# Kernel tuning notes

Hardware: AMD Instinct MI355X
Metric: run time of the kernel (lower is better)

The kernel has to match this reference:

```python
import jax, jax.numpy as jnp
import numpy as np

EPS = 1e-5

def _bn(x, gamma, beta):
    # BatchNorm1d in training mode: batch stats with biased variance
    m = jnp.mean(x, axis=0)
    v = jnp.mean((x - m) ** 2, axis=0)
    return (x - m) * jax.lax.rsqrt(v + EPS) * gamma + beta

def setup_inputs() -> dict:
    key = jax.random.key(0)
    ks = jax.random.split(key, 10)
    E, G = 500000, 512
    D_NODE, D_EDGE, D_U, OUT = 128, 64, 64, 256
    D_IN = 2 * D_NODE + D_EDGE + D_U  # 384
    return {
        "src": jax.random.normal(ks[0], (E, D_NODE), jnp.float32),
        "dest": jax.random.normal(ks[1], (E, D_NODE), jnp.float32),
        "edge_attr": jax.random.normal(ks[2], (E, D_EDGE), jnp.float32),
        "u": jax.random.normal(ks[3], (G, D_U), jnp.float32),
        "batch": jax.random.randint(ks[4], (E,), 0, G, jnp.int64),
        "W1": jax.random.normal(ks[5], (D_IN, OUT), jnp.float32) * (1.0 / np.sqrt(D_IN)),
        "g1": jnp.ones((OUT,), jnp.float32),
        "b1": jnp.zeros((OUT,), jnp.float32),
        "W2": jax.random.normal(ks[6], (OUT, OUT), jnp.float32) * (1.0 / np.sqrt(OUT)),
        "g2": jnp.ones((OUT,), jnp.float32),
        "b2": jnp.zeros((OUT,), jnp.float32),
    }

def reference(src, dest, edge_attr, u, batch, W1, g1, b1, W2, g2, b2):
    # gather per-graph globals to edges, concat features: [E, 384]
    h = jnp.concatenate([src, dest, edge_attr, u[batch]], axis=1)
    h = jax.nn.relu(_bn(h @ W1, g1, b1))  # LinearNorm + ReLU
    return _bn(h @ W2, g2, b2)            # LinearNorm
```

## Files before the change

kernel.cpp:

```cpp
#include <hip/hip_runtime.h>
#include <stdint.h>

typedef __attribute__((ext_vector_type(8))) short short8;
typedef __attribute__((ext_vector_type(4))) float float4v;

#define BM 128
#define BN 128
#define BK 32
#define LDT 40

__device__ __forceinline__ unsigned short f2bf(float f) {
    union { float f; unsigned u; } x; x.f = f;
    unsigned u = x.u;
    u += 0x7fffu + ((u >> 16) & 1u);
    return (unsigned short)(u >> 16);
}
__device__ __forceinline__ float bf2f(unsigned short s) {
    union { unsigned u; float f; } x; x.u = ((unsigned)s) << 16;
    return x.f;
}

__global__ __launch_bounds__(256) void transpose_bf16_kernel(
    const float* __restrict__ W, unsigned short* __restrict__ WT, int K, int N)
{
    int idx = blockIdx.x * 256 + threadIdx.x;
    if (idx < K * N) {
        int k = idx / N, n = idx - k * N;
        WT[(size_t)n * K + k] = f2bf(W[idx]);
    }
}

__global__ __launch_bounds__(256) void gemm1_kernel(
    const float* __restrict__ src, const float* __restrict__ dst,
    const float* __restrict__ edge, const float* __restrict__ u,
    const int* __restrict__ batch, const unsigned short* __restrict__ W1T,
    unsigned short* __restrict__ H1, float* __restrict__ psum,
    float* __restrict__ psq, int E, int MT)
{
    __shared__ __align__(16) unsigned short lsA[BM * LDT];
    __shared__ __align__(16) unsigned short lsB[BN * LDT];
    __shared__ int lsBatch[BM];
    __shared__ float ldsS[4][64];
    __shared__ float ldsQ[4][64];

    const int t = threadIdx.x;
    const int bm = blockIdx.x, bn = blockIdx.y;
    const int lane = t & 63, w = t >> 6;
    const int wm = w >> 1, wn = w & 1;
    const int quad = lane >> 4, l16 = lane & 15;

    if (t < BM) {
        int grow = bm * BM + t; if (grow >= E) grow = E - 1;
        lsBatch[t] = batch[grow];
    }

    float4v acc[4][4] = {};

    const int tc = t & 7, tr0 = t >> 3;
    const int kq = (t & 3) * 8, nb = t >> 2;
    const int n0 = bn * BN;

    for (int kk = 0; kk < 12; kk++) {
        const int kc = kk * BK;
        #pragma unroll
        for (int i = 0; i < 4; i++) {
            int rl = tr0 + 32 * i;
            int grow = bm * BM + rl; if (grow >= E) grow = E - 1;
            const float* p;
            if (kk < 4)       p = src  + (size_t)grow * 128 + kc + tc * 4;
            else if (kk < 8)  p = dst  + (size_t)grow * 128 + (kc - 128) + tc * 4;
            else if (kk < 10) p = edge + (size_t)grow * 64  + (kc - 256) + tc * 4;
            else              p = u + (size_t)lsBatch[rl] * 64 + (kc - 320) + tc * 4;
            float4v v = *(const float4v*)p;
            unsigned short* dp = &lsA[rl * LDT + tc * 4];
            dp[0] = f2bf(v[0]); dp[1] = f2bf(v[1]); dp[2] = f2bf(v[2]); dp[3] = f2bf(v[3]);
        }
        #pragma unroll
        for (int i = 0; i < 2; i++) {
            int n = nb + 64 * i;
            short8 v = *(const short8*)(W1T + (size_t)(n0 + n) * 384 + kc + kq);
            *(short8*)&lsB[n * LDT + kq] = v;
        }
        __syncthreads();
        short8 af[4], bfv[4];
        #pragma unroll
        for (int x = 0; x < 4; x++) {
            af[x]  = *(const short8*)&lsA[(wm * 64 + x * 16 + l16) * LDT + quad * 8];
            bfv[x] = *(const short8*)&lsB[(wn * 64 + x * 16 + l16) * LDT + quad * 8];
        }
        #pragma unroll
        for (int i = 0; i < 4; i++)
            #pragma unroll
            for (int j = 0; j < 4; j++)
                acc[i][j] = __builtin_amdgcn_mfma_f32_16x16x32_bf16(af[i], bfv[j], acc[i][j], 0, 0, 0);
        __syncthreads();
    }

    float s[4] = {0.f,0.f,0.f,0.f}, q[4] = {0.f,0.f,0.f,0.f};
    #pragma unroll
    for (int i = 0; i < 4; i++) {
        #pragma unroll
        for (int r = 0; r < 4; r++) {
            int row = bm * BM + wm * 64 + i * 16 + quad * 4 + r;
            bool ok = row < E;
            #pragma unroll
            for (int j = 0; j < 4; j++) {
                float v = acc[i][j][r];
                int col = bn * BN + wn * 64 + j * 16 + l16;
                if (ok) {
                    H1[(size_t)row * 256 + col] = f2bf(v);
                    s[j] += v; q[j] += v * v;
                }
            }
        }
    }
    #pragma unroll
    for (int j = 0; j < 4; j++) {
        s[j] += __shfl_xor(s[j], 16, 64); s[j] += __shfl_xor(s[j], 32, 64);
        q[j] += __shfl_xor(q[j], 16, 64); q[j] += __shfl_xor(q[j], 32, 64);
    }
    if (quad == 0) {
        #pragma unroll
        for (int j = 0; j < 4; j++) { ldsS[w][j * 16 + l16] = s[j]; ldsQ[w][j * 16 + l16] = q[j]; }
    }
    __syncthreads();
    if (t < 128) {
        int g = t >> 6, i = t & 63;
        float S = ldsS[g][i] + ldsS[g + 2][i];
        float Q = ldsQ[g][i] + ldsQ[g + 2][i];
        int col = bn * BN + t;
        psum[(size_t)col * MT + bm] = S;
        psq [(size_t)col * MT + bm] = Q;
    }
}

__global__ __launch_bounds__(256) void stats_kernel(
    const float* __restrict__ psum, const float* __restrict__ psq,
    const float* __restrict__ gamma, const float* __restrict__ beta,
    float* __restrict__ ad, int MT, float invE)
{
    __shared__ float rs[4], rq[4];
    int c = blockIdx.x;
    float s = 0.f, q = 0.f;
    for (int i = threadIdx.x; i < MT; i += 256) {
        s += psum[(size_t)c * MT + i];
        q += psq [(size_t)c * MT + i];
    }
    for (int off = 32; off >= 1; off >>= 1) {
        s += __shfl_xor(s, off, 64);
        q += __shfl_xor(q, off, 64);
    }
    int lane = threadIdx.x & 63, w = threadIdx.x >> 6;
    if (lane == 0) { rs[w] = s; rq[w] = q; }
    __syncthreads();
    if (threadIdx.x == 0) {
        float S = rs[0] + rs[1] + rs[2] + rs[3];
        float Q = rq[0] + rq[1] + rq[2] + rq[3];
        float m = S * invE;
        float v = Q * invE - m * m;
        float a = gamma[c] * rsqrtf(v + 1e-5f);
        ad[c] = a;
        ad[256 + c] = beta[c] - m * a;
    }
}

__global__ __launch_bounds__(256) void gemm2_kernel(
    const unsigned short* __restrict__ H1, const unsigned short* __restrict__ W2T,
    const float* __restrict__ ad1, float* __restrict__ out,
    float* __restrict__ psum, float* __restrict__ psq, int E, int MT)
{
    __shared__ __align__(16) unsigned short lsA[BM * LDT];
    __shared__ __align__(16) unsigned short lsB[BN * LDT];
    __shared__ float ldsS[4][64];
    __shared__ float ldsQ[4][64];

    const int t = threadIdx.x;
    const int bm = blockIdx.x, bn = blockIdx.y;
    const int lane = t & 63, w = t >> 6;
    const int wm = w >> 1, wn = w & 1;
    const int quad = lane >> 4, l16 = lane & 15;

    float4v acc[4][4] = {};

    const int kq = (t & 3) * 8, rb = t >> 2;
    const int n0 = bn * BN;

    for (int kk = 0; kk < 8; kk++) {
        const int kc = kk * BK;
        float4v aLo = *(const float4v*)(ad1 + kc + kq);
        float4v aHi = *(const float4v*)(ad1 + kc + kq + 4);
        float4v dLo = *(const float4v*)(ad1 + 256 + kc + kq);
        float4v dHi = *(const float4v*)(ad1 + 256 + kc + kq + 4);
        #pragma unroll
        for (int i = 0; i < 2; i++) {
            int rl = rb + 64 * i;
            int grow = bm * BM + rl; if (grow >= E) grow = E - 1;
            short8 hv = *(const short8*)(H1 + (size_t)grow * 256 + kc + kq);
            short8 yv;
            #pragma unroll
            for (int e = 0; e < 4; e++) {
                float y = fmaxf(fmaf(bf2f((unsigned short)hv[e]), aLo[e], dLo[e]), 0.f);
                yv[e] = (short)f2bf(y);
            }
            #pragma unroll
            for (int e = 0; e < 4; e++) {
                float y = fmaxf(fmaf(bf2f((unsigned short)hv[4 + e]), aHi[e], dHi[e]), 0.f);
                yv[4 + e] = (short)f2bf(y);
            }
            *(short8*)&lsA[rl * LDT + kq] = yv;
        }
        #pragma unroll
        for (int i = 0; i < 2; i++) {
            int n = rb + 64 * i;
            short8 v = *(const short8*)(W2T + (size_t)(n0 + n) * 256 + kc + kq);
            *(short8*)&lsB[n * LDT + kq] = v;
        }
        __syncthreads();
        short8 af[4], bfv[4];
        #pragma unroll
        for (int x = 0; x < 4; x++) {
            af[x]  = *(const short8*)&lsA[(wm * 64 + x * 16 + l16) * LDT + quad * 8];
            bfv[x] = *(const short8*)&lsB[(wn * 64 + x * 16 + l16) * LDT + quad * 8];
        }
        #pragma unroll
        for (int i = 0; i < 4; i++)
            #pragma unroll
            for (int j = 0; j < 4; j++)
                acc[i][j] = __builtin_amdgcn_mfma_f32_16x16x32_bf16(af[i], bfv[j], acc[i][j], 0, 0, 0);
        __syncthreads();
    }

    float s[4] = {0.f,0.f,0.f,0.f}, q[4] = {0.f,0.f,0.f,0.f};
    #pragma unroll
    for (int i = 0; i < 4; i++) {
        #pragma unroll
        for (int r = 0; r < 4; r++) {
            int row = bm * BM + wm * 64 + i * 16 + quad * 4 + r;
            bool ok = row < E;
            #pragma unroll
            for (int j = 0; j < 4; j++) {
                float v = acc[i][j][r];
                int col = bn * BN + wn * 64 + j * 16 + l16;
                if (ok) {
                    out[(size_t)row * 256 + col] = v;
                    s[j] += v; q[j] += v * v;
                }
            }
        }
    }
    #pragma unroll
    for (int j = 0; j < 4; j++) {
        s[j] += __shfl_xor(s[j], 16, 64); s[j] += __shfl_xor(s[j], 32, 64);
        q[j] += __shfl_xor(q[j], 16, 64); q[j] += __shfl_xor(q[j], 32, 64);
    }
    if (quad == 0) {
        #pragma unroll
        for (int j = 0; j < 4; j++) { ldsS[w][j * 16 + l16] = s[j]; ldsQ[w][j * 16 + l16] = q[j]; }
    }
    __syncthreads();
    if (t < 128) {
        int g = t >> 6, i = t & 63;
        float S = ldsS[g][i] + ldsS[g + 2][i];
        float Q = ldsQ[g][i] + ldsQ[g + 2][i];
        int col = bn * BN + t;
        psum[(size_t)col * MT + bm] = S;
        psq [(size_t)col * MT + bm] = Q;
    }
}

__global__ __launch_bounds__(256) void finalize_kernel(
    float* __restrict__ out, const float* __restrict__ ad, long n4)
{
    long stride = (long)gridDim.x * 256;
    for (long i = (long)blockIdx.x * 256 + threadIdx.x; i < n4; i += stride) {
        float4v v = ((float4v*)out)[i];
        int c4 = (int)(i & 63);
        float4v a = ((const float4v*)ad)[c4];
        float4v d = ((const float4v*)(ad + 256))[c4];
        v = a * v + d;
        ((float4v*)out)[i] = v;
    }
}

extern "C" void kernel_launch(void* const* d_in, const int* in_sizes, int n_in,
                              void* d_out, int out_size, void* d_ws, size_t ws_size,
                              hipStream_t stream)
{
    const float* src  = (const float*)d_in[0];
    const float* dst  = (const float*)d_in[1];
    const float* edge = (const float*)d_in[2];
    const float* u    = (const float*)d_in[3];
    const int*   batch= (const int*)d_in[4];
    const float* W1   = (const float*)d_in[5];
    const float* g1   = (const float*)d_in[6];
    const float* b1   = (const float*)d_in[7];
    const float* W2   = (const float*)d_in[8];
    const float* g2   = (const float*)d_in[9];
    const float* b2   = (const float*)d_in[10];
    float* out = (float*)d_out;

    const int E  = in_sizes[0] / 128;
    const int MT = (E + BM - 1) / BM;

    char* ws = (char*)d_ws;
    size_t off = 0;
    auto alloc = [&](size_t bytes) -> void* {
        void* p = (void*)(ws + off);
        off += (bytes + 255) & ~(size_t)255;
        return p;
    };
    unsigned short* H1  = (unsigned short*)alloc((size_t)E * 256 * 2);
    unsigned short* W1T = (unsigned short*)alloc((size_t)256 * 384 * 2);
    unsigned short* W2T = (unsigned short*)alloc((size_t)256 * 256 * 2);
    float* psum = (float*)alloc((size_t)256 * MT * 4);
    float* psq  = (float*)alloc((size_t)256 * MT * 4);
    float* ad1  = (float*)alloc(512 * 4);
    float* ad2  = (float*)alloc(512 * 4);
    (void)ws_size; (void)n_in; (void)out_size;

    transpose_bf16_kernel<<<(384 * 256 + 255) / 256, 256, 0, stream>>>(W1, W1T, 384, 256);
    transpose_bf16_kernel<<<(256 * 256 + 255) / 256, 256, 0, stream>>>(W2, W2T, 256, 256);
    gemm1_kernel<<<dim3(MT, 2), 256, 0, stream>>>(src, dst, edge, u, batch, W1T, H1, psum, psq, E, MT);
    stats_kernel<<<256, 256, 0, stream>>>(psum, psq, g1, b1, ad1, MT, 1.0f / (float)E);
    gemm2_kernel<<<dim3(MT, 2), 256, 0, stream>>>(H1, W2T, ad1, out, psum, psq, E, MT);
    stats_kernel<<<256, 256, 0, stream>>>(psum, psq, g2, b2, ad2, MT, 1.0f / (float)E);
    const long n4 = (long)E * 64;
    finalize_kernel<<<16384, 256, 0, stream>>>(out, ad2, n4);
}
```

Measured before the change: 1.525 ms.

## Double-buffer A tiles and load B fragments directly from global in both GEMMs

Both GEMM kernels now prefetch the next K-slice of A (and W) into registers while MFMAs run on the current slice. The A tile sits in a double-buffered LDS array, so only one barrier per iteration is needed instead of two. The B operand no longer goes through LDS: each wave reads its MFMA fragments straight from global memory. A-tile stores are packed into 64-bit writes. This hides global-load latency behind compute, at the cost of more registers and uncoalesced, repeated per-wave global reads of the weights.

New measurement: 1.607 ms. 5.4% more time.

```diff
diff --git a/kernel.cpp b/kernel.cpp
--- a/kernel.cpp
+++ b/kernel.cpp
@@ -3,6 +3,7 @@
 
 typedef __attribute__((ext_vector_type(8))) short short8;
 typedef __attribute__((ext_vector_type(4))) float float4v;
+typedef __attribute__((ext_vector_type(2))) unsigned int uint2v;
 
 #define BM 128
 #define BN 128
@@ -37,8 +38,7 @@
     unsigned short* __restrict__ H1, float* __restrict__ psum,
     float* __restrict__ psq, int E, int MT)
 {
-    __shared__ __align__(16) unsigned short lsA[BM * LDT];
-    __shared__ __align__(16) unsigned short lsB[BN * LDT];
+    __shared__ __align__(16) unsigned short lsA[2][BM * LDT];
     __shared__ int lsBatch[BM];
     __shared__ float ldsS[4][64];
     __shared__ float ldsQ[4][64];
@@ -57,43 +57,78 @@
     float4v acc[4][4] = {};
 
     const int tc = t & 7, tr0 = t >> 3;
-    const int kq = (t & 3) * 8, nb = t >> 2;
     const int n0 = bn * BN;
-
+    const unsigned short* Bbase = W1T + (size_t)(n0 + wn * 64 + l16) * 384 + quad * 8;
+
+    float4v aCur[4]; short8 bCur[4];
+
+    #pragma unroll
+    for (int i = 0; i < 4; i++) {
+        int rl = tr0 + 32 * i;
+        int grow = bm * BM + rl; if (grow >= E) grow = E - 1;
+        aCur[i] = *(const float4v*)(src + (size_t)grow * 128 + tc * 4);
+    }
+    #pragma unroll
+    for (int x = 0; x < 4; x++)
+        bCur[x] = *(const short8*)(Bbase + (size_t)x * 16 * 384);
+    #pragma unroll
+    for (int i = 0; i < 4; i++) {
+        int rl = tr0 + 32 * i;
+        unsigned lo = (unsigned)f2bf(aCur[i][0]) | ((unsigned)f2bf(aCur[i][1]) << 16);
+        unsigned hi = (unsigned)f2bf(aCur[i][2]) | ((unsigned)f2bf(aCur[i][3]) << 16);
+        uint2v v2; v2.x = lo; v2.y = hi;
+        *(uint2v*)&lsA[0][rl * LDT + tc * 4] = v2;
+    }
+    __syncthreads();
+
+    int cur = 0;
+    #pragma unroll 1
     for (int kk = 0; kk < 12; kk++) {
-        const int kc = kk * BK;
-        #pragma unroll
-        for (int i = 0; i < 4; i++) {
-            int rl = tr0 + 32 * i;
-            int grow = bm * BM + rl; if (grow >= E) grow = E - 1;
-            const float* p;
-            if (kk < 4)       p = src  + (size_t)grow * 128 + kc + tc * 4;
-            else if (kk < 8)  p = dst  + (size_t)grow * 128 + (kc - 128) + tc * 4;
-            else if (kk < 10) p = edge + (size_t)grow * 64  + (kc - 256) + tc * 4;
-            else              p = u + (size_t)lsBatch[rl] * 64 + (kc - 320) + tc * 4;
-            float4v v = *(const float4v*)p;
-            unsigned short* dp = &lsA[rl * LDT + tc * 4];
-            dp[0] = f2bf(v[0]); dp[1] = f2bf(v[1]); dp[2] = f2bf(v[2]); dp[3] = f2bf(v[3]);
-        }
-        #pragma unroll
-        for (int i = 0; i < 2; i++) {
-            int n = nb + 64 * i;
-            short8 v = *(const short8*)(W1T + (size_t)(n0 + n) * 384 + kc + kq);
-            *(short8*)&lsB[n * LDT + kq] = v;
-        }
-        __syncthreads();
-        short8 af[4], bfv[4];
-        #pragma unroll
-        for (int x = 0; x < 4; x++) {
-            af[x]  = *(const short8*)&lsA[(wm * 64 + x * 16 + l16) * LDT + quad * 8];
-            bfv[x] = *(const short8*)&lsB[(wn * 64 + x * 16 + l16) * LDT + quad * 8];
-        }
+        float4v aN[4]; short8 bN[4];
+        const bool pf = (kk < 11);
+        if (pf) {
+            const int k1 = kk + 1;
+            const int kc2 = k1 * BK;
+            const float* base; int rstride, coff;
+            bool isU = false;
+            if (k1 < 4)       { base = src;  rstride = 128; coff = kc2; }
+            else if (k1 < 8)  { base = dst;  rstride = 128; coff = kc2 - 128; }
+            else if (k1 < 10) { base = edge; rstride = 64;  coff = kc2 - 256; }
+            else              { base = u;    rstride = 64;  coff = kc2 - 320; isU = true; }
+            #pragma unroll
+            for (int i = 0; i < 4; i++) {
+                int rl = tr0 + 32 * i;
+                int grow = bm * BM + rl; if (grow >= E) grow = E - 1;
+                int r = isU ? lsBatch[rl] : grow;
+                aN[i] = *(const float4v*)(base + (size_t)r * rstride + coff + tc * 4);
+            }
+            #pragma unroll
+            for (int x = 0; x < 4; x++)
+                bN[x] = *(const short8*)(Bbase + (size_t)x * 16 * 384 + kc2);
+        }
+        short8 af[4];
+        #pragma unroll
+        for (int x = 0; x < 4; x++)
+            af[x] = *(const short8*)&lsA[cur][(wm * 64 + x * 16 + l16) * LDT + quad * 8];
         #pragma unroll
         for (int i = 0; i < 4; i++)
             #pragma unroll
             for (int j = 0; j < 4; j++)
-                acc[i][j] = __builtin_amdgcn_mfma_f32_16x16x32_bf16(af[i], bfv[j], acc[i][j], 0, 0, 0);
-        __syncthreads();
+                acc[i][j] = __builtin_amdgcn_mfma_f32_16x16x32_bf16(af[i], bCur[j], acc[i][j], 0, 0, 0);
+        if (pf) {
+            #pragma unroll
+            for (int i = 0; i < 4; i++) {
+                int rl = tr0 + 32 * i;
+                unsigned lo = (unsigned)f2bf(aN[i][0]) | ((unsigned)f2bf(aN[i][1]) << 16);
+                unsigned hi = (unsigned)f2bf(aN[i][2]) | ((unsigned)f2bf(aN[i][3]) << 16);
+                uint2v v2; v2.x = lo; v2.y = hi;
+                *(uint2v*)&lsA[cur ^ 1][rl * LDT + tc * 4] = v2;
+            }
+            #pragma unroll
+            for (int x = 0; x < 4; x++) bCur[x] = bN[x];
+            cur ^= 1;
+            __syncthreads();
+        }
     }
 
     float s[4] = {0.f,0.f,0.f,0.f}, q[4] = {0.f,0.f,0.f,0.f};
@@ -169,8 +204,7 @@
     const float* __restrict__ ad1, float* __restrict__ out,
     float* __restrict__ psum, float* __restrict__ psq, int E, int MT)
 {
-    __shared__ __align__(16) unsigned short lsA[BM * LDT];
-    __shared__ __align__(16) unsigned short lsB[BN * LDT];
+    __shared__ __align__(16) unsigned short lsA[2][BM * LDT];
     __shared__ float ldsS[4][64];
     __shared__ float ldsQ[4][64];
 
@@ -184,50 +218,93 @@
 
     const int kq = (t & 3) * 8, rb = t >> 2;
     const int n0 = bn * BN;
-
+    const unsigned short* Bbase = W2T + (size_t)(n0 + wn * 64 + l16) * 256 + quad * 8;
+
+    short8 hCur[2]; float4v adC[4]; short8 bCur[4];
+
+    adC[0] = *(const float4v*)(ad1 + kq);
+    adC[1] = *(const float4v*)(ad1 + kq + 4);
+    adC[2] = *(const float4v*)(ad1 + 256 + kq);
+    adC[3] = *(const float4v*)(ad1 + 256 + kq + 4);
+    #pragma unroll
+    for (int i = 0; i < 2; i++) {
+        int rl = rb + 64 * i;
+        int grow = bm * BM + rl; if (grow >= E) grow = E - 1;
+        hCur[i] = *(const short8*)(H1 + (size_t)grow * 256 + kq);
+    }
+    #pragma unroll
+    for (int x = 0; x < 4; x++)
+        bCur[x] = *(const short8*)(Bbase + (size_t)x * 16 * 256);
+    #pragma unroll
+    for (int i = 0; i < 2; i++) {
+        int rl = rb + 64 * i;
+        short8 yv;
+        #pragma unroll
+        for (int e = 0; e < 4; e++) {
+            float y = fmaxf(fmaf(bf2f((unsigned short)hCur[i][e]), adC[0][e], adC[2][e]), 0.f);
+            yv[e] = (short)f2bf(y);
+        }
+        #pragma unroll
+        for (int e = 0; e < 4; e++) {
+            float y = fmaxf(fmaf(bf2f((unsigned short)hCur[i][4 + e]), adC[1][e], adC[3][e]), 0.f);
+            yv[4 + e] = (short)f2bf(y);
+        }
+        *(short8*)&lsA[0][rl * LDT + kq] = yv;
+    }
+    __syncthreads();
+
+    int cur = 0;
+    #pragma unroll 1
     for (int kk = 0; kk < 8; kk++) {
-        const int kc = kk * BK;
-        float4v aLo = *(const float4v*)(ad1 + kc + kq);
-        float4v aHi = *(const float4v*)(ad1 + kc + kq + 4);
-        float4v dLo = *(const float4v*)(ad1 + 256 + kc + kq);
-        float4v dHi = *(const float4v*)(ad1 + 256 + kc + kq + 4);
-        #pragma unroll
-        for (int i = 0; i < 2; i++) {
-            int rl = rb + 64 * i;
-            int grow = bm * BM + rl; if (grow >= E) grow = E - 1;
-            short8 hv = *(const short8*)(H1 + (size_t)grow * 256 + kc + kq);
-            short8 yv;
-            #pragma unroll
-            for (int e = 0; e < 4; e++) {
-                float y = fmaxf(fmaf(bf2f((unsigned short)hv[e]), aLo[e], dLo[e]), 0.f);
-                yv[e] = (short)f2bf(y);
-            }
-            #pragma unroll
-            for (int e = 0; e < 4; e++) {
-                float y = fmaxf(fmaf(bf2f((unsigned short)hv[4 + e]), aHi[e], dHi[e]), 0.f);
-                yv[4 + e] = (short)f2bf(y);
-            }
-            *(short8*)&lsA[rl * LDT + kq] = yv;
-        }
-        #pragma unroll
-        for (int i = 0; i < 2; i++) {
-            int n = rb + 64 * i;
-            short8 v = *(const short8*)(W2T + (size_t)(n0 + n) * 256 + kc + kq);
-            *(short8*)&lsB[n * LDT + kq] = v;
-        }
-        __syncthreads();
-        short8 af[4], bfv[4];
-        #pragma unroll
-        for (int x = 0; x < 4; x++) {
-            af[x]  = *(const short8*)&lsA[(wm * 64 + x * 16 + l16) * LDT + quad * 8];
-            bfv[x] = *(const short8*)&lsB[(wn * 64 + x * 16 + l16) * LDT + quad * 8];
-        }
+        short8 hN[2]; float4v adN[4]; short8 bN[4];
+        const bool pf = (kk < 7);
+        if (pf) {
+            const int kc2 = (kk + 1) * BK;
+            adN[0] = *(const float4v*)(ad1 + kc2 + kq);
+            adN[1] = *(const float4v*)(ad1 + kc2 + kq + 4);
+            adN[2] = *(const float4v*)(ad1 + 256 + kc2 + kq);
+            adN[3] = *(const float4v*)(ad1 + 256 + kc2 + kq + 4);
+            #pragma unroll
+            for (int i = 0; i < 2; i++) {
+                int rl = rb + 64 * i;
+                int grow = bm * BM + rl; if (grow >= E) grow = E - 1;
+                hN[i] = *(const short8*)(H1 + (size_t)grow * 256 + kc2 + kq);
+            }
+            #pragma unroll
+            for (int x = 0; x < 4; x++)
+                bN[x] = *(const short8*)(Bbase + (size_t)x * 16 * 256 + kc2);
+        }
+        short8 af[4];
+        #pragma unroll
+        for (int x = 0; x < 4; x++)
+            af[x] = *(const short8*)&lsA[cur][(wm * 64 + x * 16 + l16) * LDT + quad * 8];
         #pragma unroll
         for (int i = 0; i < 4; i++)
             #pragma unroll
             for (int j = 0; j < 4; j++)
-                acc[i][j] = __builtin_amdgcn_mfma_f32_16x16x32_bf16(af[i], bfv[j], acc[i][j], 0, 0, 0);
-        __syncthreads();
+                acc[i][j] = __builtin_amdgcn_mfma_f32_16x16x32_bf16(af[i], bCur[j], acc[i][j], 0, 0, 0);
+        if (pf) {
+            #pragma unroll
+            for (int i = 0; i < 2; i++) {
+                int rl = rb + 64 * i;
+                short8 yv;
+                #pragma unroll
+                for (int e = 0; e < 4; e++) {
+                    float y = fmaxf(fmaf(bf2f((unsigned short)hN[i][e]), adN[0][e], adN[2][e]), 0.f);
+                    yv[e] = (short)f2bf(y);
+                }
+                #pragma unroll
+                for (int e = 0; e < 4; e++) {
+                    float y = fmaxf(fmaf(bf2f((unsigned short)hN[i][4 + e]), adN[1][e], adN[3][e]), 0.f);
+                    yv[4 + e] = (short)f2bf(y);
+                }
+                *(short8*)&lsA[cur ^ 1][rl * LDT + kq] = yv;
+            }
+            #pragma unroll
+            for (int x = 0; x < 4; x++) bCur[x] = bN[x];
+            cur ^= 1;
+            __syncthreads();
+        }
     }
 
     float s[4] = {0.f,0.f,0.f,0.f}, q[4] = {0.f,0.f,0.f,0.f};
```
